# Kernel tuning notes

Hardware: AMD Instinct MI355X
Metric: run time of the kernel (lower is better)

The kernel has to match this reference:

```python
import math
import jax, jax.numpy as jnp
import numpy as np

EMBED_LEN = 512  # self.dk in the torch module (used for scaling, NOT the head dim)


def setup_inputs() -> dict:
    key = jax.random.key(0)
    kq, kk, kv = jax.random.split(key, 3)
    B, H, S, D = 2, 8, 4096, 64
    queries = jax.random.normal(kq, (B, H, S, D), dtype=jnp.float32)
    keys = jax.random.normal(kk, (B, H, S, D), dtype=jnp.float32)
    # NOTE: values enters as [B, S, H, D]; forward transposes dims (1,2).
    values = jax.random.normal(kv, (B, S, H, D), dtype=jnp.float32)
    return {"queries": queries, "keys": keys, "values": values}


def reference(queries, keys, values):
    # compatibility = Q @ K^T / sqrt(dk), dk = embed_len (512), mask=None branch
    scores = jnp.einsum("bhqd,bhkd->bhqk", queries, keys) / math.sqrt(EMBED_LEN)
    attn = jax.nn.softmax(scores, axis=3)
    # torch.transpose(values, 1, 2): [B,S,H,D] -> [B,H,S,D]
    v = jnp.swapaxes(values, 1, 2)
    return jnp.einsum("bhqk,bhkd->bhqd", attn, v)
```

## Files before the change

kernel.cpp:

```cpp
#include <hip/hip_runtime.h>

typedef __attribute__((ext_vector_type(8))) short bf16x8;
typedef __attribute__((ext_vector_type(4))) short s16x4;
typedef __attribute__((ext_vector_type(4))) float f32x4;

#define MFMA16 __builtin_amdgcn_mfma_f32_16x16x32_bf16

#if __has_builtin(__builtin_amdgcn_exp2f)
__device__ __forceinline__ float exp2_raw(float x) { return __builtin_amdgcn_exp2f(x); }
#else
__device__ __forceinline__ float exp2_raw(float x) {
    float r;
    asm volatile("v_exp_f32 %0, %1" : "=v"(r) : "v"(x));
    return r;
}
#endif

__device__ __forceinline__ short bf16s(float f) {
    __bf16 h = (__bf16)f;
    return __builtin_bit_cast(short, h);
}

__device__ __forceinline__ void gload16(const char* g, char* l) {
    __builtin_amdgcn_global_load_lds(
        (const __attribute__((address_space(1))) unsigned int*)g,
        (__attribute__((address_space(3))) unsigned int*)l, 16, 0, 0);
}

__global__ __launch_bounds__(256) void prep_k(const float* __restrict__ K,
                                              char* __restrict__ Kimg) {
    const int bid = blockIdx.x;
    const int t = threadIdx.x;
    const int c = t & 3, r = t >> 2;
    char* dst = Kimg + (size_t)bid * 8192;
    const float* src = K + (size_t)bid * 4096 + (size_t)r * 64 + c * 16;
    float e[16];
    *(float4*)(e)      = *(const float4*)(src);
    *(float4*)(e + 4)  = *(const float4*)(src + 4);
    *(float4*)(e + 8)  = *(const float4*)(src + 8);
    *(float4*)(e + 12) = *(const float4*)(src + 12);
#pragma unroll
    for (int lg = 0; lg < 4; ++lg) {
        s16x4 wv;
#pragma unroll
        for (int j = 0; j < 4; ++j) wv[j] = bf16s(e[lg * 4 + j]);
        const unsigned f = (unsigned)((((c >> 1) * 4 + lg) ^ (r & 7)));
        *(s16x4*)(dst + r * 128 + f * 16 + (c & 1) * 8) = wv;
    }
}

__global__ __launch_bounds__(256) void prep_v(const float* __restrict__ V,
                                              char* __restrict__ Vimg) {
    const int bid = blockIdx.x;
    const int head = bid >> 6, it = bid & 63;
    const int b = head >> 3, h = head & 7;
    const int t = threadIdx.x;
    const int d = t & 63, f0 = t >> 6;
    char* dst = Vimg + (size_t)bid * 8192;
#pragma unroll
    for (int ff = 0; ff < 2; ++ff) {
        const int f = f0 + ff * 4;
        const int hh = f >> 2, lg = f & 3;
        const int kv0 = hh * 32 + lg * 4;
        const float* src = V + ((size_t)b * 4096 + it * 64 + kv0) * 512 + h * 64 + d;
        bf16x8 wv;
#pragma unroll
        for (int j = 0; j < 4; ++j) wv[j]     = bf16s(src[(size_t)j * 512]);
#pragma unroll
        for (int j = 0; j < 4; ++j) wv[4 + j] = bf16s(src[(size_t)(16 + j) * 512]);
        *(bf16x8*)(dst + d * 128 + (unsigned)((f ^ (d & 7)) * 16)) = wv;
    }
}

__global__ __launch_bounds__(64, 2)
void sdpa_fa_kernel(const float* __restrict__ Q, const char* __restrict__ Kimg,
                    const char* __restrict__ Vimg, float* __restrict__ O) {
    __shared__ __align__(16) char LDS[32768];

    const int bid  = blockIdx.x;
    const int xcd  = bid & 7;
    const int idx  = bid >> 3;
    const int head = xcd + 8 * (idx >> 6);
    const int qt   = idx & 63;
    const int hb   = head * 64;

    const int l   = threadIdx.x;
    const int lg  = l >> 4;
    const int lc  = l & 15;
    const int lc7 = lc & 7;

    const float C1 = (float)(1.4426950408889634 / 22.627416997969522);

    bf16x8 qf[4][2];
#pragma unroll
    for (int qi = 0; qi < 4; ++qi) {
        const int qrow = qt * 64 + qi * 16 + lc;
        const float* qp = Q + ((size_t)head * 4096 + qrow) * 64;
#pragma unroll
        for (int half = 0; half < 2; ++half) {
            bf16x8 f;
#pragma unroll
            for (int j = 0; j < 4; ++j) {
                f[j]     = bf16s(qp[half * 32 + lg * 4 + j] * C1);
                f[4 + j] = bf16s(qp[half * 32 + 16 + lg * 4 + j] * C1);
            }
            qf[qi][half] = f;
        }
    }

    bf16x8 ones;
#pragma unroll
    for (int j = 0; j < 8; ++j) ones[j] = (short)0x3F80;

    f32x4 Oa[4][4];
    f32x4 ls[4];
#pragma unroll
    for (int qi = 0; qi < 4; ++qi) {
        ls[qi] = (f32x4){0.f, 0.f, 0.f, 0.f};
#pragma unroll
        for (int dt = 0; dt < 4; ++dt) Oa[qi][dt] = (f32x4){0.f, 0.f, 0.f, 0.f};
    }

    auto stage = [&](int it, int buf) {
        const char* gk = Kimg + (size_t)(hb + it) * 8192 + l * 16;
        const char* gv = Vimg + (size_t)(hb + it) * 8192 + l * 16;
        char* lk = LDS + buf * 16384;
        char* lv = LDS + buf * 16384 + 8192;
#pragma unroll
        for (int i = 0; i < 8; ++i) gload16(gk + i * 1024, lk + i * 1024);
#pragma unroll
        for (int i = 0; i < 8; ++i) gload16(gv + i * 1024, lv + i * 1024);
    };

    auto body = [&](const char* Kb, const char* Vb, int nextit, int nextbuf) {
        asm volatile("s_waitcnt vmcnt(0)" ::: "memory");
        __builtin_amdgcn_sched_barrier(0);

        bf16x8 kf[4][2];
#pragma unroll
        for (int g = 0; g < 4; ++g) {
            const unsigned ro = (unsigned)((g * 16 + lc) * 128);
            kf[g][0] = *(const bf16x8*)(Kb + ro + (unsigned)(((0 + lg) ^ lc7) * 16));
            kf[g][1] = *(const bf16x8*)(Kb + ro + (unsigned)(((4 + lg) ^ lc7) * 16));
        }
        bf16x8 vf[4][2];
#pragma unroll
        for (int dt = 0; dt < 4; ++dt) {
            const unsigned ro = (unsigned)((dt * 16 + lc) * 128);
            vf[dt][0] = *(const bf16x8*)(Vb + ro + (unsigned)(((0 + lg) ^ lc7) * 16));
            vf[dt][1] = *(const bf16x8*)(Vb + ro + (unsigned)(((4 + lg) ^ lc7) * 16));
        }
        __builtin_amdgcn_sched_barrier(0);

        if (nextit >= 0) stage(nextit, nextbuf);
        __builtin_amdgcn_sched_barrier(0);

        f32x4 st0[4][2], st1[4][2];
#pragma unroll
        for (int g2 = 0; g2 < 2; ++g2)
#pragma unroll
            for (int qi = 0; qi < 4; ++qi) {
                f32x4 a = (f32x4){0.f, 0.f, 0.f, 0.f};
                a = MFMA16(kf[g2][0], qf[qi][0], a, 0, 0, 0);
                a = MFMA16(kf[g2][1], qf[qi][1], a, 0, 0, 0);
                st0[qi][g2] = a;
            }

#pragma unroll
        for (int g2 = 0; g2 < 2; ++g2)
#pragma unroll
            for (int qi = 0; qi < 4; ++qi) {
                f32x4 a = (f32x4){0.f, 0.f, 0.f, 0.f};
                a = MFMA16(kf[g2 + 2][0], qf[qi][0], a, 0, 0, 0);
                a = MFMA16(kf[g2 + 2][1], qf[qi][1], a, 0, 0, 0);
                st1[qi][g2] = a;
#pragma unroll
                for (int r = 0; r < 4; ++r) st0[qi][g2][r] = exp2_raw(st0[qi][g2][r]);
            }
        bf16x8 pfr0[4];
#pragma unroll
        for (int qi = 0; qi < 4; ++qi) {
            bf16x8 f;
#pragma unroll
            for (int j = 0; j < 4; ++j) {
                f[j]     = bf16s(st0[qi][0][j]);
                f[4 + j] = bf16s(st0[qi][1][j]);
            }
            pfr0[qi] = f;
        }

#pragma unroll
        for (int qi = 0; qi < 4; ++qi) {
            ls[qi] = MFMA16(pfr0[qi], ones, ls[qi], 0, 0, 0);
#pragma unroll
            for (int r = 0; r < 4; ++r) st1[qi][0][r] = exp2_raw(st1[qi][0][r]);
            Oa[qi][0] = MFMA16(pfr0[qi], vf[0][0], Oa[qi][0], 0, 0, 0);
            Oa[qi][1] = MFMA16(pfr0[qi], vf[1][0], Oa[qi][1], 0, 0, 0);
#pragma unroll
            for (int r = 0; r < 4; ++r) st1[qi][1][r] = exp2_raw(st1[qi][1][r]);
            Oa[qi][2] = MFMA16(pfr0[qi], vf[2][0], Oa[qi][2], 0, 0, 0);
            Oa[qi][3] = MFMA16(pfr0[qi], vf[3][0], Oa[qi][3], 0, 0, 0);
        }
        bf16x8 pfr1[4];
#pragma unroll
        for (int qi = 0; qi < 4; ++qi) {
            bf16x8 f;
#pragma unroll
            for (int j = 0; j < 4; ++j) {
                f[j]     = bf16s(st1[qi][0][j]);
                f[4 + j] = bf16s(st1[qi][1][j]);
            }
            pfr1[qi] = f;
        }

#pragma unroll
        for (int qi = 0; qi < 4; ++qi) {
            ls[qi] = MFMA16(pfr1[qi], ones, ls[qi], 0, 0, 0);
#pragma unroll
            for (int dt = 0; dt < 4; ++dt)
                Oa[qi][dt] = MFMA16(pfr1[qi], vf[dt][1], Oa[qi][dt], 0, 0, 0);
        }
    };

    stage(0, 0);

#pragma unroll 1
    for (int itp = 0; itp < 32; ++itp) {
        const int it0 = itp * 2;
        body(LDS, LDS + 8192, it0 + 1, 1);
        body(LDS + 16384, LDS + 16384 + 8192,
             (it0 + 2 < 64) ? (it0 + 2) : -1, 0);
    }

#pragma unroll
    for (int qi = 0; qi < 4; ++qi) {
#pragma unroll
        for (int r = 0; r < 4; ++r) {
            const float inv = 1.0f / ls[qi][r];
            const int q = qt * 64 + qi * 16 + lg * 4 + r;
            float* og = O + ((size_t)head * 4096 + q) * 64 + lc;
#pragma unroll
            for (int dt = 0; dt < 4; ++dt) og[dt * 16] = Oa[qi][dt][r] * inv;
        }
    }
}

extern "C" void kernel_launch(void* const* d_in, const int* in_sizes, int n_in,
                              void* d_out, int out_size, void* d_ws, size_t ws_size,
                              hipStream_t stream) {
    const float* Q = (const float*)d_in[0];
    const float* K = (const float*)d_in[1];
    const float* V = (const float*)d_in[2];
    float* Out = (float*)d_out;
    char* Kimg = (char*)d_ws;
    char* Vimg = (char*)d_ws + (size_t)8388608;
    prep_k<<<dim3(1024), dim3(256), 0, stream>>>(K, Kimg);
    prep_v<<<dim3(1024), dim3(256), 0, stream>>>(V, Vimg);
    sdpa_fa_kernel<<<dim3(1024), dim3(64), 0, stream>>>(Q, Kimg, Vimg, Out);
}
```

Measured before the change: 91.14 us.

## Split KV sequence across two blocks per query tile and merge partials

Each attention block now processes half of the KV sequence, doubling the grid to 2048 single-wave blocks. Unnormalized partial outputs and row sums are written to the output buffer and a workspace, then a new merge kernel adds them and normalizes. LDS drops to a single 16KB buffer with an explicit LDS wait before the next prefetch, replacing the double buffer. This is meant to improve occupancy and CU fill, at the cost of an extra launch, extra global traffic for the partials, and less overlap between loading and compute.

Result: slower. 93.90 us (+3.0%).

```diff
diff --git a/kernel.cpp b/kernel.cpp
--- a/kernel.cpp
+++ b/kernel.cpp
@@ -74,15 +74,17 @@
 
 __global__ __launch_bounds__(64, 2)
 void sdpa_fa_kernel(const float* __restrict__ Q, const char* __restrict__ Kimg,
-                    const char* __restrict__ Vimg, float* __restrict__ O) {
-    __shared__ __align__(16) char LDS[32768];
+                    const char* __restrict__ Vimg, float* __restrict__ P0,
+                    float* __restrict__ P1, float* __restrict__ LS) {
+    __shared__ __align__(16) char LDS[16384];
 
     const int bid  = blockIdx.x;
     const int xcd  = bid & 7;
     const int idx  = bid >> 3;
-    const int head = xcd + 8 * (idx >> 6);
+    const int head = xcd + 8 * (idx >> 7);
+    const int kvh  = (idx >> 6) & 1;
     const int qt   = idx & 63;
-    const int hb   = head * 64;
+    const int hb   = head * 64 + kvh * 32;
 
     const int l   = threadIdx.x;
     const int lg  = l >> 4;
@@ -121,18 +123,19 @@
         for (int dt = 0; dt < 4; ++dt) Oa[qi][dt] = (f32x4){0.f, 0.f, 0.f, 0.f};
     }
 
-    auto stage = [&](int it, int buf) {
+    auto stage = [&](int it) {
         const char* gk = Kimg + (size_t)(hb + it) * 8192 + l * 16;
         const char* gv = Vimg + (size_t)(hb + it) * 8192 + l * 16;
-        char* lk = LDS + buf * 16384;
-        char* lv = LDS + buf * 16384 + 8192;
-#pragma unroll
-        for (int i = 0; i < 8; ++i) gload16(gk + i * 1024, lk + i * 1024);
-#pragma unroll
-        for (int i = 0; i < 8; ++i) gload16(gv + i * 1024, lv + i * 1024);
+#pragma unroll
+        for (int i = 0; i < 8; ++i) gload16(gk + i * 1024, LDS + i * 1024);
+#pragma unroll
+        for (int i = 0; i < 8; ++i) gload16(gv + i * 1024, LDS + 8192 + i * 1024);
     };
 
-    auto body = [&](const char* Kb, const char* Vb, int nextit, int nextbuf) {
+    stage(0);
+
+#pragma unroll 1
+    for (int it = 0; it < 32; ++it) {
         asm volatile("s_waitcnt vmcnt(0)" ::: "memory");
         __builtin_amdgcn_sched_barrier(0);
 
@@ -140,19 +143,20 @@
 #pragma unroll
         for (int g = 0; g < 4; ++g) {
             const unsigned ro = (unsigned)((g * 16 + lc) * 128);
-            kf[g][0] = *(const bf16x8*)(Kb + ro + (unsigned)(((0 + lg) ^ lc7) * 16));
-            kf[g][1] = *(const bf16x8*)(Kb + ro + (unsigned)(((4 + lg) ^ lc7) * 16));
+            kf[g][0] = *(const bf16x8*)(LDS + ro + (unsigned)(((0 + lg) ^ lc7) * 16));
+            kf[g][1] = *(const bf16x8*)(LDS + ro + (unsigned)(((4 + lg) ^ lc7) * 16));
         }
         bf16x8 vf[4][2];
 #pragma unroll
         for (int dt = 0; dt < 4; ++dt) {
-            const unsigned ro = (unsigned)((dt * 16 + lc) * 128);
-            vf[dt][0] = *(const bf16x8*)(Vb + ro + (unsigned)(((0 + lg) ^ lc7) * 16));
-            vf[dt][1] = *(const bf16x8*)(Vb + ro + (unsigned)(((4 + lg) ^ lc7) * 16));
-        }
+            const unsigned ro = (unsigned)(8192 + (dt * 16 + lc) * 128);
+            vf[dt][0] = *(const bf16x8*)(LDS + ro + (unsigned)(((0 + lg) ^ lc7) * 16));
+            vf[dt][1] = *(const bf16x8*)(LDS + ro + (unsigned)(((4 + lg) ^ lc7) * 16));
+        }
+        asm volatile("s_waitcnt lgkmcnt(0)" ::: "memory");
         __builtin_amdgcn_sched_barrier(0);
 
-        if (nextit >= 0) stage(nextit, nextbuf);
+        if (it + 1 < 32) stage(it + 1);
         __builtin_amdgcn_sched_barrier(0);
 
         f32x4 st0[4][2], st1[4][2];
@@ -220,29 +224,37 @@
             for (int dt = 0; dt < 4; ++dt)
                 Oa[qi][dt] = MFMA16(pfr1[qi], vf[dt][1], Oa[qi][dt], 0, 0, 0);
         }
-    };
-
-    stage(0, 0);
-
-#pragma unroll 1
-    for (int itp = 0; itp < 32; ++itp) {
-        const int it0 = itp * 2;
-        body(LDS, LDS + 8192, it0 + 1, 1);
-        body(LDS + 16384, LDS + 16384 + 8192,
-             (it0 + 2 < 64) ? (it0 + 2) : -1, 0);
-    }
-
+    }
+
+    float* P = kvh ? P1 : P0;
+    float* lsw = LS + kvh * 65536;
 #pragma unroll
     for (int qi = 0; qi < 4; ++qi) {
 #pragma unroll
         for (int r = 0; r < 4; ++r) {
-            const float inv = 1.0f / ls[qi][r];
             const int q = qt * 64 + qi * 16 + lg * 4 + r;
-            float* og = O + ((size_t)head * 4096 + q) * 64 + lc;
-#pragma unroll
-            for (int dt = 0; dt < 4; ++dt) og[dt * 16] = Oa[qi][dt][r] * inv;
-        }
-    }
+            float* og = P + ((size_t)head * 4096 + q) * 64 + lc;
+#pragma unroll
+            for (int dt = 0; dt < 4; ++dt) og[dt * 16] = Oa[qi][dt][r];
+            if (lc == 0) lsw[head * 4096 + q] = ls[qi][r];
+        }
+    }
+}
+
+__global__ __launch_bounds__(256) void merge_out(const float* __restrict__ P1,
+                                                 const float* __restrict__ LS,
+                                                 float* __restrict__ Out) {
+    const int i = (blockIdx.x * 256 + threadIdx.x) * 4;
+    const int hq = i >> 6;
+    const float inv = 1.0f / (LS[hq] + LS[65536 + hq]);
+    const float4 a = *(const float4*)(Out + i);
+    const float4 b = *(const float4*)(P1 + i);
+    float4 r;
+    r.x = (a.x + b.x) * inv;
+    r.y = (a.y + b.y) * inv;
+    r.z = (a.z + b.z) * inv;
+    r.w = (a.w + b.w) * inv;
+    *(float4*)(Out + i) = r;
 }
 
 extern "C" void kernel_launch(void* const* d_in, const int* in_sizes, int n_in,
@@ -254,7 +266,10 @@
     float* Out = (float*)d_out;
     char* Kimg = (char*)d_ws;
     char* Vimg = (char*)d_ws + (size_t)8388608;
+    float* P1  = (float*)((char*)d_ws + (size_t)16777216);
+    float* LS  = (float*)((char*)d_ws + (size_t)33554432);
     prep_k<<<dim3(1024), dim3(256), 0, stream>>>(K, Kimg);
     prep_v<<<dim3(1024), dim3(256), 0, stream>>>(V, Vimg);
-    sdpa_fa_kernel<<<dim3(1024), dim3(64), 0, stream>>>(Q, Kimg, Vimg, Out);
-}
+    sdpa_fa_kernel<<<dim3(2048), dim3(64), 0, stream>>>(Q, Kimg, Vimg, Out, P1, LS);
+    merge_out<<<dim3(4096), dim3(256), 0, stream>>>(P1, LS, Out);
+}
```
